# Kernel optimization log

Measured on AMD Instinct MI355X. Metric: run time of the kernel, lower is better.

Reference implementation:

```python
import jax, jax.numpy as jnp
import numpy as np

N, E, F_IN, D, H, G, T = 30000, 480000, 128, 32, 4, 128, 10
HD = H * D
NEG_SLOPE = 0.2


def _lin(key, fan_out, fan_in, scale=0.05):
    k1, k2 = jax.random.split(key)
    return (jax.random.normal(k1, (fan_out, fan_in), jnp.float32) * scale,
            jax.random.normal(k2, (fan_out,), jnp.float32) * scale)


def setup_inputs() -> dict:
    key = jax.random.key(0)
    ks = jax.random.split(key, 24)
    x = jax.random.normal(ks[0], (N, F_IN), jnp.float32)
    edge_index = jax.random.randint(ks[1], (2, E), 0, N, jnp.int64)
    batch = jnp.sort(jax.random.randint(ks[2], (N,), 0, G, jnp.int64))
    inp = {"x": x, "edge_index": edge_index, "batch": batch}
    # conv 0 (in=F_IN) and conv 1 (in=D); each followed by Linear(HD -> D)
    for i, fin in enumerate([F_IN, D]):
        base = 3 + i * 8
        Wl, bl = _lin(ks[base + 0], HD, fin)
        Wr, br = _lin(ks[base + 1], HD, fin)
        att = jax.random.normal(ks[base + 2], (H, D), jnp.float32) * 0.05
        bias = jnp.zeros((HD,), jnp.float32)
        lw, lb = _lin(ks[base + 3], D, HD)
        inp.update({f"Wl{i}": Wl, f"bl{i}": bl, f"Wr{i}": Wr, f"br{i}": br,
                    f"att{i}": att, f"cb{i}": bias, f"lw{i}": lw, f"lb{i}": lb})
    inp["fc1_W"], inp["fc1_b"] = _lin(ks[20], D, D)
    inp["fc2_W"], inp["fc2_b"] = _lin(ks[21], T, D)
    return inp


def _gatv2_conv(x, src, dst, Wl, bl, Wr, br, att, bias):
    # PyG GATv2Conv, concat=True, add_self_loops already applied to src/dst,
    # aggr='mean', eval mode (no dropout).
    n = x.shape[0]
    xl = (x @ Wl.T + bl).reshape(n, H, D)
    xr = (x @ Wr.T + br).reshape(n, H, D)
    e = jax.nn.leaky_relu(xl[src] + xr[dst], NEG_SLOPE)          # [E', H, D]
    alpha = jnp.einsum('ehd,hd->eh', e, att)                      # [E', H]
    amax = jax.ops.segment_max(alpha, dst, num_segments=n)        # [n, H]
    ex = jnp.exp(alpha - amax[dst])
    denom = jax.ops.segment_sum(ex, dst, num_segments=n)
    a = ex / denom[dst]                                           # softmax per target
    msg = xl[src] * a[:, :, None]                                 # [E', H, D]
    s = jax.ops.segment_sum(msg, dst, num_segments=n)
    cnt = jax.ops.segment_sum(jnp.ones((src.shape[0],), jnp.float32), dst, num_segments=n)
    out = s / cnt[:, None, None]                                  # mean aggregation
    return out.reshape(n, HD) + bias


def reference(x, edge_index, batch,
              Wl0, bl0, Wr0, br0, att0, cb0, lw0, lb0,
              Wl1, bl1, Wr1, br1, att1, cb1, lw1, lb1,
              fc1_W, fc1_b, fc2_W, fc2_b):
    loop = jnp.arange(N, dtype=edge_index.dtype)
    src = jnp.concatenate([edge_index[0], loop])  # add self loops
    dst = jnp.concatenate([edge_index[1], loop])
    convs = [(Wl0, bl0, Wr0, br0, att0, cb0, lw0, lb0),
             (Wl1, bl1, Wr1, br1, att1, cb1, lw1, lb1)]
    h = x
    for (Wl, bl, Wr, br, att, cb, lw, lb) in convs:
        h = _gatv2_conv(h, src, dst, Wl, bl, Wr, br, att, cb)
        h = h @ lw.T + lb  # heads>1: Linear(H*D -> D)
    g = jax.ops.segment_max(h, batch, num_segments=G)  # global max pool
    g = jax.nn.relu(g @ fc1_W.T + fc1_b)
    return g @ fc2_W.T + fc2_b
```

## Files before the change

### kernel.cpp

```cpp
#include <hip/hip_runtime.h>
#include <hip/hip_bf16.h>

#define NEG_SLOPE 0.2f
#define GGRP 128
#define TOUT 10

__global__ void init_kernel(int* __restrict__ deg, float* __restrict__ gpool,
                            int n, int gsize) {
    int i = blockIdx.x * blockDim.x + threadIdx.x;
    if (i < n) deg[i] = 0;
    if (i < gsize) gpool[i] = -__builtin_inff();
}

__global__ void degree_kernel(const int* __restrict__ dst, int* __restrict__ deg, int E) {
    int e = blockIdx.x * blockDim.x + threadIdx.x;
    if (e < E) atomicAdd(&deg[dst[e]], 1);
}

__global__ __launch_bounds__(256)
void scanA_kernel(const int* __restrict__ deg, int* __restrict__ rowptr,
                  int* __restrict__ bsum, int n) {
    __shared__ int wsum[4];
    int tid = threadIdx.x, lane = tid & 63, wid = tid >> 6;
    int idx = blockIdx.x * 256 + tid;
    int v = (idx < n) ? deg[idx] : 0;
    int x = v;
    #pragma unroll
    for (int off = 1; off < 64; off <<= 1) {
        int t = __shfl_up(x, off, 64);
        if (lane >= off) x += t;
    }
    if (lane == 63) wsum[wid] = x;
    __syncthreads();
    if (tid == 0) {
        int s = 0;
        #pragma unroll
        for (int i = 0; i < 4; ++i) { int t = wsum[i]; wsum[i] = s; s += t; }
        bsum[blockIdx.x] = s;
    }
    __syncthreads();
    int excl = x - v + wsum[wid];
    if (idx < n) rowptr[idx] = excl;
}

__global__ void scanB_kernel(const int* __restrict__ bsum, int* __restrict__ boff,
                             int* __restrict__ rowptr, int n, int nb) {
    int lane = threadIdx.x;
    int v0 = (lane < nb) ? bsum[lane] : 0;
    int v1 = (64 + lane < nb) ? bsum[64 + lane] : 0;
    int s0 = v0, s1 = v1;
    #pragma unroll
    for (int off = 1; off < 64; off <<= 1) {
        int t0 = __shfl_up(s0, off, 64);
        int t1 = __shfl_up(s1, off, 64);
        if (lane >= off) { s0 += t0; s1 += t1; }
    }
    int tot0 = __shfl(s0, 63, 64);
    s1 += tot0;
    boff[lane] = s0 - v0;
    boff[64 + lane] = s1 - v1;
    if (lane == 63) rowptr[n] = s1;
}

__global__ void scanC_kernel(int* __restrict__ rowptr, int* __restrict__ cursor,
                             const int* __restrict__ boff, int n) {
    int idx = blockIdx.x * blockDim.x + threadIdx.x;
    if (idx < n) {
        int r = rowptr[idx] + boff[idx >> 8];
        rowptr[idx] = r;
        cursor[idx] = r;
    }
}

__global__ void scatter_kernel(const int* __restrict__ src, const int* __restrict__ dst,
                               int* __restrict__ cursor, int* __restrict__ csr, int E) {
    int e = blockIdx.x * blockDim.x + threadIdx.x;
    if (e < E) {
        int slot = atomicAdd(&cursor[dst[e]], 1);
        csr[slot] = src[e];
    }
}

template <int FIN>
__global__ __launch_bounds__(256)
void gemm_xlxr_kernel(const float* __restrict__ X,
                      const float* __restrict__ Wl, const float* __restrict__ bl,
                      const float* __restrict__ Wr, const float* __restrict__ br,
                      float* __restrict__ xl, float* __restrict__ xr) {
    __shared__ float Wls[128][36];
    __shared__ float Wrs[128][36];
    __shared__ float Xs[16][36];
    int tid = threadIdx.x;
    int rowBase = blockIdx.x * 16;
    int c = tid & 127;
    int rs = tid >> 7;
    float accL[8] = {0.f}, accR[8] = {0.f};
    for (int k0 = 0; k0 < FIN; k0 += 32) {
        #pragma unroll
        for (int i = 0; i < 16; ++i) {
            int idx = tid + i * 256;
            int cc = idx >> 5, kk = idx & 31;
            Wls[cc][kk] = Wl[cc * FIN + k0 + kk];
            Wrs[cc][kk] = Wr[cc * FIN + k0 + kk];
        }
        #pragma unroll
        for (int i = 0; i < 2; ++i) {
            int idx = tid + i * 256;
            int r = idx >> 5, kk = idx & 31;
            Xs[r][kk] = X[(rowBase + r) * FIN + k0 + kk];
        }
        __syncthreads();
        #pragma unroll
        for (int k4 = 0; k4 < 32; k4 += 4) {
            float4 wl4 = *(const float4*)&Wls[c][k4];
            float4 wr4 = *(const float4*)&Wrs[c][k4];
            #pragma unroll
            for (int j = 0; j < 8; ++j) {
                float4 xv = *(const float4*)&Xs[rs * 8 + j][k4];
                accL[j] = fmaf(xv.x, wl4.x, accL[j]);
                accL[j] = fmaf(xv.y, wl4.y, accL[j]);
                accL[j] = fmaf(xv.z, wl4.z, accL[j]);
                accL[j] = fmaf(xv.w, wl4.w, accL[j]);
                accR[j] = fmaf(xv.x, wr4.x, accR[j]);
                accR[j] = fmaf(xv.y, wr4.y, accR[j]);
                accR[j] = fmaf(xv.z, wr4.z, accR[j]);
                accR[j] = fmaf(xv.w, wr4.w, accR[j]);
            }
        }
        __syncthreads();
    }
    float blv = bl[c], brv = br[c];
    #pragma unroll
    for (int j = 0; j < 8; ++j) {
        int row = rowBase + rs * 8 + j;
        xl[row * 128 + c] = accL[j] + blv;
        xr[row * 128 + c] = accR[j] + brv;
    }
}

__global__ __launch_bounds__(256)
void gat_fused_kernel(const float* __restrict__ xl, const float* __restrict__ xr,
                      const float* __restrict__ att, const float* __restrict__ cb,
                      const float* __restrict__ lw, const float* __restrict__ lb,
                      const int* __restrict__ rowptr, const int* __restrict__ csr,
                      float* __restrict__ out , int n) {
    __shared__ float lws[32][132];
    __shared__ float oslot[4][128];
    int tid = threadIdx.x;
    #pragma unroll
    for (int i = 0; i < 16; ++i) {
        int idx = tid + i * 256;
        lws[idx >> 7][idx & 127] = lw[idx];
    }
    __syncthreads();

    int wid = tid >> 6, lane = tid & 63;
    int nd = blockIdx.x * 4 + wid;
    if (nd >= n) return;
    int half = lane >> 5;
    int l32 = lane & 31;
    int f4 = l32 * 4;

    const float4 xr4  = *(const float4*)(xr + nd * 128 + f4);
    const float4 at4  = *(const float4*)(att + f4);
    const float4 xls4 = *(const float4*)(xl + nd * 128 + f4);

    int start = rowptr[nd], end = rowptr[nd + 1];

    float den;
    float4 acc;
    {
        float e0 = xls4.x + xr4.x; e0 = e0 > 0.f ? e0 : NEG_SLOPE * e0;
        float e1 = xls4.y + xr4.y; e1 = e1 > 0.f ? e1 : NEG_SLOPE * e1;
        float e2 = xls4.z + xr4.z; e2 = e2 > 0.f ? e2 : NEG_SLOPE * e2;
        float e3 = xls4.w + xr4.w; e3 = e3 > 0.f ? e3 : NEG_SLOPE * e3;
        float q = e0 * at4.x + e1 * at4.y + e2 * at4.z + e3 * at4.w;
        q += __shfl_xor(q, 1); q += __shfl_xor(q, 2); q += __shfl_xor(q, 4);
        float a = __expf(q);
        if (half == 0) {
            den = a;
            acc.x = a * xls4.x; acc.y = a * xls4.y;
            acc.z = a * xls4.z; acc.w = a * xls4.w;
        } else {
            den = 0.f; acc.x = acc.y = acc.z = acc.w = 0.f;
        }
    }

    for (int i = start + half; i < end; i += 2) {
        int s = csr[i];
        float4 xv = *(const float4*)(xl + (size_t)s * 128 + f4);
        float e0 = xv.x + xr4.x; e0 = e0 > 0.f ? e0 : NEG_SLOPE * e0;
        float e1 = xv.y + xr4.y; e1 = e1 > 0.f ? e1 : NEG_SLOPE * e1;
        float e2 = xv.z + xr4.z; e2 = e2 > 0.f ? e2 : NEG_SLOPE * e2;
        float e3 = xv.w + xr4.w; e3 = e3 > 0.f ? e3 : NEG_SLOPE * e3;
        float q = e0 * at4.x + e1 * at4.y + e2 * at4.z + e3 * at4.w;
        q += __shfl_xor(q, 1); q += __shfl_xor(q, 2); q += __shfl_xor(q, 4);
        float a = __expf(q);
        den += a;
        acc.x = fmaf(a, xv.x, acc.x);
        acc.y = fmaf(a, xv.y, acc.y);
        acc.z = fmaf(a, xv.z, acc.z);
        acc.w = fmaf(a, xv.w, acc.w);
    }

    acc.x += __shfl_xor(acc.x, 32);
    acc.y += __shfl_xor(acc.y, 32);
    acc.z += __shfl_xor(acc.z, 32);
    acc.w += __shfl_xor(acc.w, 32);
    den   += __shfl_xor(den, 32);

    float inv = 1.0f / (den * (float)(end - start + 1));
    const float4 cb4 = *(const float4*)(cb + f4);
    float4 o;
    o.x = fmaf(acc.x, inv, cb4.x);
    o.y = fmaf(acc.y, inv, cb4.y);
    o.z = fmaf(acc.z, inv, cb4.z);
    o.w = fmaf(acc.w, inv, cb4.w);

    if (half == 0) *(float4*)&oslot[wid][f4] = o;
    asm volatile("s_waitcnt lgkmcnt(0)" ::: "memory");

    float y = 0.f;
    int kbase = half * 64;
    #pragma unroll
    for (int k = 0; k < 64; k += 4) {
        float4 lv = *(const float4*)&lws[l32][kbase + k];
        float4 ov = *(const float4*)&oslot[wid][kbase + k];
        y = fmaf(lv.x, ov.x, y);
        y = fmaf(lv.y, ov.y, y);
        y = fmaf(lv.z, ov.z, y);
        y = fmaf(lv.w, ov.w, y);
    }
    y += __shfl_xor(y, 32);
    if (half == 0) out[nd * 32 + l32] = y + lb[l32];
}

__device__ __forceinline__ void atomicMaxFloat(float* addr, float val) {
    if (val >= 0.f) atomicMax((int*)addr, __float_as_int(val));
    else atomicMin((unsigned int*)addr, (unsigned int)__float_as_int(val));
}

__global__ void pool_kernel(const float* __restrict__ H, const int* __restrict__ batch,
                            float* __restrict__ g, int n) {
    int tid = threadIdx.x;
    int dim = tid & 31;
    int sub = tid >> 5;
    int nodeStart = blockIdx.x * 128 + sub * 16;
    float m = -__builtin_inff();
    int cur = -1;
    for (int j = 0; j < 16; ++j) {
        int nd = nodeStart + j;
        if (nd >= n) break;
        int b = batch[nd];
        if (b != cur) {
            if (cur >= 0) atomicMaxFloat(&g[cur * 32 + dim], m);
            cur = b; m = -__builtin_inff();
        }
        m = fmaxf(m, H[nd * 32 + dim]);
    }
    if (cur >= 0) atomicMaxFloat(&g[cur * 32 + dim], m);
}

__global__ __launch_bounds__(256)
void fc_kernel(const float* __restrict__ g,
               const float* __restrict__ fc1W, const float* __restrict__ fc1b,
               const float* __restrict__ fc2W, const float* __restrict__ fc2b,
               float* __restrict__ out) {
    __shared__ float g1[GGRP * 32];
    int tid = threadIdx.x;
    for (int idx = tid; idx < GGRP * 32; idx += 256) {
        int r = idx >> 5, c = idx & 31;
        float acc = fc1b[c];
        #pragma unroll
        for (int k = 0; k < 32; ++k) acc = fmaf(g[r * 32 + k], fc1W[c * 32 + k], acc);
        g1[idx] = acc > 0.f ? acc : 0.f;
    }
    __syncthreads();
    for (int idx = tid; idx < GGRP * TOUT; idx += 256) {
        int r = idx / TOUT, c = idx - r * TOUT;
        float acc = fc2b[c];
        #pragma unroll
        for (int k = 0; k < 32; ++k) acc = fmaf(g1[r * 32 + k], fc2W[c * 32 + k], acc);
        out[idx] = acc;
    }
}

extern "C" void kernel_launch(void* const* d_in, const int* in_sizes, int n_in,
                              void* d_out, int out_size, void* d_ws, size_t ws_size,
                              hipStream_t stream) {
    const float* x     = (const float*)d_in[0];
    const int*   ei    = (const int*)d_in[1];
    const int*   batch = (const int*)d_in[2];
    const float* Wl0 = (const float*)d_in[3];
    const float* bl0 = (const float*)d_in[4];
    const float* Wr0 = (const float*)d_in[5];
    const float* br0 = (const float*)d_in[6];
    const float* at0 = (const float*)d_in[7];
    const float* cb0 = (const float*)d_in[8];
    const float* lw0 = (const float*)d_in[9];
    const float* lb0 = (const float*)d_in[10];
    const float* Wl1 = (const float*)d_in[11];
    const float* bl1 = (const float*)d_in[12];
    const float* Wr1 = (const float*)d_in[13];
    const float* br1 = (const float*)d_in[14];
    const float* at1 = (const float*)d_in[15];
    const float* cb1 = (const float*)d_in[16];
    const float* lw1 = (const float*)d_in[17];
    const float* lb1 = (const float*)d_in[18];
    const float* fc1W = (const float*)d_in[19];
    const float* fc1b = (const float*)d_in[20];
    const float* fc2W = (const float*)d_in[21];
    const float* fc2b = (const float*)d_in[22];

    const int n = in_sizes[0] / 128;
    const int E = in_sizes[1] / 2;
    const int* src = ei;
    const int* dst = ei + E;
    const int nblkScan = (n + 255) / 256;

    size_t off = 0;
    auto alloc = [&](size_t bytes) {
        void* p = (char*)d_ws + off;
        off += (bytes + 255) & ~(size_t)255;
        return p;
    };
    float* xl    = (float*)alloc((size_t)n * 128 * 4);
    float* xr    = (float*)alloc((size_t)n * 128 * 4);
    float* hbuf  = (float*)alloc((size_t)n * 32 * 4);
    int* deg     = (int*)alloc((size_t)n * 4);
    int* rowptr  = (int*)alloc((size_t)(n + 1) * 4);
    int* cursor  = (int*)alloc((size_t)n * 4);
    int* csr     = (int*)alloc((size_t)E * 4);
    int* bsum    = (int*)alloc(128 * 4);
    int* boff    = (int*)alloc(128 * 4);
    float* gpool = (float*)alloc((size_t)GGRP * 32 * 4);

    init_kernel<<<(n + 255) / 256, 256, 0, stream>>>(deg, gpool, n, GGRP * 32);
    degree_kernel<<<(E + 255) / 256, 256, 0, stream>>>(dst, deg, E);
    scanA_kernel<<<nblkScan, 256, 0, stream>>>(deg, rowptr, bsum, n);
    scanB_kernel<<<1, 64, 0, stream>>>(bsum, boff, rowptr, n, nblkScan);
    scanC_kernel<<<nblkScan, 256, 0, stream>>>(rowptr, cursor, boff, n);
    scatter_kernel<<<(E + 255) / 256, 256, 0, stream>>>(src, dst, cursor, csr, E);

    gemm_xlxr_kernel<128><<<n / 16, 256, 0, stream>>>(x, Wl0, bl0, Wr0, br0, xl, xr);
    gat_fused_kernel<<<(n + 3) / 4, 256, 0, stream>>>(xl, xr, at0, cb0, lw0, lb0,
                                                      rowptr, csr, hbuf, n);
    gemm_xlxr_kernel<32><<<n / 16, 256, 0, stream>>>(hbuf, Wl1, bl1, Wr1, br1, xl, xr);
    gat_fused_kernel<<<(n + 3) / 4, 256, 0, stream>>>(xl, xr, at1, cb1, lw1, lb1,
                                                      rowptr, csr, hbuf, n);

    pool_kernel<<<(n + 127) / 128, 256, 0, stream>>>(hbuf, batch, gpool, n);
    fc_kernel<<<1, 256, 0, stream>>>(gpool, fc1W, fc1b, fc2W, fc2b, (float*)d_out);
}
```

Before: 345.2 us.

## Retile xl/xr GEMM into column blocks and prefetch neighbor gathers in GAT

```diff
diff --git a/kernel.cpp b/kernel.cpp
--- a/kernel.cpp
+++ b/kernel.cpp
@@ -86,55 +86,53 @@
 void gemm_xlxr_kernel(const float* __restrict__ X,
                       const float* __restrict__ Wl, const float* __restrict__ bl,
                       const float* __restrict__ Wr, const float* __restrict__ br,
-                      float* __restrict__ xl, float* __restrict__ xr) {
-    __shared__ float Wls[128][36];
-    __shared__ float Wrs[128][36];
-    __shared__ float Xs[16][36];
+                      float* __restrict__ xl, float* __restrict__ xr, int n) {
+    constexpr int KP = FIN + 4;
+    __shared__ float Ws[64][KP];
+    __shared__ float Xs[32][KP];
     int tid = threadIdx.x;
-    int rowBase = blockIdx.x * 16;
-    int c = tid & 127;
-    int rs = tid >> 7;
-    float accL[8] = {0.f}, accR[8] = {0.f};
-    for (int k0 = 0; k0 < FIN; k0 += 32) {
+    int nRowBlk = (n + 31) >> 5;
+    int rowBlk = blockIdx.x % nRowBlk;
+    int colBlk = blockIdx.x / nRowBlk;
+    const float* Wbase = (colBlk < 2) ? Wl : Wr;
+    const float* bbase = (colBlk < 2) ? bl : br;
+    float*       obase = (colBlk < 2) ? xl : xr;
+    int cOff = (colBlk & 1) * 64;
+    int row0 = rowBlk * 32;
+
+    for (int idx = tid * 4; idx < 64 * FIN; idx += 1024) {
+        int r = idx / FIN, k = idx % FIN;
+        *(float4*)&Ws[r][k] = *(const float4*)&Wbase[(cOff + r) * FIN + k];
+    }
+    for (int idx = tid * 4; idx < 32 * FIN; idx += 1024) {
+        int r = idx / FIN, k = idx % FIN;
+        int gr = row0 + r;
+        float4 v = {0.f, 0.f, 0.f, 0.f};
+        if (gr < n) v = *(const float4*)&X[(size_t)gr * FIN + k];
+        *(float4*)&Xs[r][k] = v;
+    }
+    __syncthreads();
+
+    int cc = tid & 63;
+    int rg = tid >> 6;
+    float acc[8] = {0.f, 0.f, 0.f, 0.f, 0.f, 0.f, 0.f, 0.f};
+    #pragma unroll 4
+    for (int k = 0; k < FIN; k += 4) {
+        float4 w4 = *(const float4*)&Ws[cc][k];
         #pragma unroll
-        for (int i = 0; i < 16; ++i) {
-            int idx = tid + i * 256;
-            int cc = idx >> 5, kk = idx & 31;
-            Wls[cc][kk] = Wl[cc * FIN + k0 + kk];
-            Wrs[cc][kk] = Wr[cc * FIN + k0 + kk];
+        for (int j = 0; j < 8; ++j) {
+            float4 x4 = *(const float4*)&Xs[rg * 8 + j][k];
+            acc[j] = fmaf(x4.x, w4.x, acc[j]);
+            acc[j] = fmaf(x4.y, w4.y, acc[j]);
+            acc[j] = fmaf(x4.z, w4.z, acc[j]);
+            acc[j] = fmaf(x4.w, w4.w, acc[j]);
         }
-        #pragma unroll
-        for (int i = 0; i < 2; ++i) {
-            int idx = tid + i * 256;
-            int r = idx >> 5, kk = idx & 31;
-            Xs[r][kk] = X[(rowBase + r) * FIN + k0 + kk];
-        }
-        __syncthreads();
-        #pragma unroll
-        for (int k4 = 0; k4 < 32; k4 += 4) {
-            float4 wl4 = *(const float4*)&Wls[c][k4];
-            float4 wr4 = *(const float4*)&Wrs[c][k4];
-            #pragma unroll
-            for (int j = 0; j < 8; ++j) {
-                float4 xv = *(const float4*)&Xs[rs * 8 + j][k4];
-                accL[j] = fmaf(xv.x, wl4.x, accL[j]);
-                accL[j] = fmaf(xv.y, wl4.y, accL[j]);
-                accL[j] = fmaf(xv.z, wl4.z, accL[j]);
-                accL[j] = fmaf(xv.w, wl4.w, accL[j]);
-                accR[j] = fmaf(xv.x, wr4.x, accR[j]);
-                accR[j] = fmaf(xv.y, wr4.y, accR[j]);
-                accR[j] = fmaf(xv.z, wr4.z, accR[j]);
-                accR[j] = fmaf(xv.w, wr4.w, accR[j]);
-            }
-        }
-        __syncthreads();
-    }
-    float blv = bl[c], brv = br[c];
+    }
+    float bv = bbase[cOff + cc];
     #pragma unroll
     for (int j = 0; j < 8; ++j) {
-        int row = rowBase + rs * 8 + j;
-        xl[row * 128 + c] = accL[j] + blv;
-        xr[row * 128 + c] = accR[j] + brv;
+        int gr = row0 + rg * 8 + j;
+        if (gr < n) obase[(size_t)gr * 128 + cOff + cc] = acc[j] + bv;
     }
 }
 
@@ -161,9 +159,9 @@
     int l32 = lane & 31;
     int f4 = l32 * 4;
 
-    const float4 xr4  = *(const float4*)(xr + nd * 128 + f4);
+    const float4 xr4  = *(const float4*)(xr + (size_t)nd * 128 + f4);
     const float4 at4  = *(const float4*)(att + f4);
-    const float4 xls4 = *(const float4*)(xl + nd * 128 + f4);
+    const float4 xls4 = *(const float4*)(xl + (size_t)nd * 128 + f4);
 
     int start = rowptr[nd], end = rowptr[nd + 1];
 
@@ -186,9 +184,16 @@
         }
     }
 
-    for (int i = start + half; i < end; i += 2) {
-        int s = csr[i];
-        float4 xv = *(const float4*)(xl + (size_t)s * 128 + f4);
+    int i = start + half;
+    int sA = (i < end) ? csr[i] : 0;
+    int sB = (i + 2 < end) ? csr[i + 2] : 0;
+    float4 xvA = {0.f, 0.f, 0.f, 0.f};
+    if (i < end) xvA = *(const float4*)(xl + (size_t)sA * 128 + f4);
+    for (; i < end; i += 2) {
+        float4 xv = xvA;
+        sA = sB;
+        if (i + 4 < end) sB = csr[i + 4];
+        if (i + 2 < end) xvA = *(const float4*)(xl + (size_t)sA * 128 + f4);
         float e0 = xv.x + xr4.x; e0 = e0 > 0.f ? e0 : NEG_SLOPE * e0;
         float e1 = xv.y + xr4.y; e1 = e1 > 0.f ? e1 : NEG_SLOPE * e1;
         float e2 = xv.z + xr4.z; e2 = e2 > 0.f ? e2 : NEG_SLOPE * e2;
@@ -232,7 +237,7 @@
         y = fmaf(lv.w, ov.w, y);
     }
     y += __shfl_xor(y, 32);
-    if (half == 0) out[nd * 32 + l32] = y + lb[l32];
+    if (half == 0) out[(size_t)nd * 32 + l32] = y + lb[l32];
 }
 
 __device__ __forceinline__ void atomicMaxFloat(float* addr, float val) {
@@ -317,6 +322,7 @@
     const int* src = ei;
     const int* dst = ei + E;
     const int nblkScan = (n + 255) / 256;
+    const int nRowBlk = (n + 31) / 32;
 
     size_t off = 0;
     auto alloc = [&](size_t bytes) {
@@ -342,10 +348,10 @@
     scanC_kernel<<<nblkScan, 256, 0, stream>>>(rowptr, cursor, boff, n);
     scatter_kernel<<<(E + 255) / 256, 256, 0, stream>>>(src, dst, cursor, csr, E);
 
-    gemm_xlxr_kernel<128><<<n / 16, 256, 0, stream>>>(x, Wl0, bl0, Wr0, br0, xl, xr);
+    gemm_xlxr_kernel<128><<<4 * nRowBlk, 256, 0, stream>>>(x, Wl0, bl0, Wr0, br0, xl, xr, n);
     gat_fused_kernel<<<(n + 3) / 4, 256, 0, stream>>>(xl, xr, at0, cb0, lw0, lb0,
                                                       rowptr, csr, hbuf, n);
-    gemm_xlxr_kernel<32><<<n / 16, 256, 0, stream>>>(hbuf, Wl1, bl1, Wr1, br1, xl, xr);
+    gemm_xlxr_kernel<32><<<4 * nRowBlk, 256, 0, stream>>>(hbuf, Wl1, bl1, Wr1, br1, xl, xr, n);
     gat_fused_kernel<<<(n + 3) / 4, 256, 0, stream>>>(xl, xr, at1, cb1, lw1, lb1,
                                                       rowptr, csr, hbuf, n);
 
```

New measurement: 346.8 us. About the same (+0.5%).

## Use 128x128 register-tiled GEMM and 4-way edge-parallel prefetching GAT aggregation

Applied to the files above, without the earlier changes.

```diff
diff --git a/kernel.cpp b/kernel.cpp
--- a/kernel.cpp
+++ b/kernel.cpp
@@ -82,59 +82,104 @@
 }
 
 template <int FIN>
-__global__ __launch_bounds__(256)
-void gemm_xlxr_kernel(const float* __restrict__ X,
+__global__ __launch_bounds__(256, 2)
+void gemm_tile_kernel(const float* __restrict__ X,
                       const float* __restrict__ Wl, const float* __restrict__ bl,
                       const float* __restrict__ Wr, const float* __restrict__ br,
-                      float* __restrict__ xl, float* __restrict__ xr) {
-    __shared__ float Wls[128][36];
-    __shared__ float Wrs[128][36];
-    __shared__ float Xs[16][36];
+                      float* __restrict__ xl, float* __restrict__ xr,
+                      int n, int nRowBlk) {
+    constexpr int BK = 32, BM = 128, LDA = BM + 4;
+    constexpr int NCHUNK = FIN / BK;
+    __shared__ float Xs[BK][LDA];
+    __shared__ float Ws[BK][LDA];
     int tid = threadIdx.x;
-    int rowBase = blockIdx.x * 16;
-    int c = tid & 127;
-    int rs = tid >> 7;
-    float accL[8] = {0.f}, accR[8] = {0.f};
-    for (int k0 = 0; k0 < FIN; k0 += 32) {
-        #pragma unroll
-        for (int i = 0; i < 16; ++i) {
-            int idx = tid + i * 256;
-            int cc = idx >> 5, kk = idx & 31;
-            Wls[cc][kk] = Wl[cc * FIN + k0 + kk];
-            Wrs[cc][kk] = Wr[cc * FIN + k0 + kk];
-        }
-        #pragma unroll
-        for (int i = 0; i < 2; ++i) {
-            int idx = tid + i * 256;
-            int r = idx >> 5, kk = idx & 31;
-            Xs[r][kk] = X[(rowBase + r) * FIN + k0 + kk];
-        }
-        __syncthreads();
-        #pragma unroll
-        for (int k4 = 0; k4 < 32; k4 += 4) {
-            float4 wl4 = *(const float4*)&Wls[c][k4];
-            float4 wr4 = *(const float4*)&Wrs[c][k4];
+    int rowBlk = blockIdx.x;
+    int colBlk = 0;
+    if (rowBlk >= nRowBlk) { rowBlk -= nRowBlk; colBlk = 1; }
+    const float* __restrict__ Wb = colBlk ? Wr : Wl;
+    const float* __restrict__ bb = colBlk ? br : bl;
+    float* __restrict__ ob = colBlk ? xr : xl;
+    int row0 = rowBlk * BM;
+
+    int sr  = tid >> 3;
+    int skq = (tid & 7) * 4;
+
+    float4 xpre[4], wpre[4];
+
+    auto load_pre = [&](int c) {
+        int k0 = c * BK;
+        #pragma unroll
+        for (int i = 0; i < 4; ++i) {
+            int r = sr + i * 32;
+            int gr = row0 + r;
+            float4 v = {0.f, 0.f, 0.f, 0.f};
+            if (gr < n) v = *(const float4*)&X[(size_t)gr * FIN + k0 + skq];
+            xpre[i] = v;
+            wpre[i] = *(const float4*)&Wb[(size_t)r * FIN + k0 + skq];
+        }
+    };
+    auto store_pre = [&]() {
+        #pragma unroll
+        for (int i = 0; i < 4; ++i) {
+            int r = sr + i * 32;
+            Xs[skq + 0][r] = xpre[i].x; Xs[skq + 1][r] = xpre[i].y;
+            Xs[skq + 2][r] = xpre[i].z; Xs[skq + 3][r] = xpre[i].w;
+            Ws[skq + 0][r] = wpre[i].x; Ws[skq + 1][r] = wpre[i].y;
+            Ws[skq + 2][r] = wpre[i].z; Ws[skq + 3][r] = wpre[i].w;
+        }
+    };
+
+    load_pre(0);
+    store_pre();
+    __syncthreads();
+
+    int tx = tid & 15;
+    int ty = tid >> 4;
+    float acc[8][8];
+    #pragma unroll
+    for (int i = 0; i < 8; ++i)
+        #pragma unroll
+        for (int j = 0; j < 8; ++j) acc[i][j] = 0.f;
+
+    #pragma unroll
+    for (int c = 0; c < NCHUNK; ++c) {
+        if (c + 1 < NCHUNK) load_pre(c + 1);
+        #pragma unroll 8
+        for (int k = 0; k < BK; ++k) {
+            float4 a0 = *(const float4*)&Xs[k][ty * 8];
+            float4 a1 = *(const float4*)&Xs[k][ty * 8 + 4];
+            float4 b0 = *(const float4*)&Ws[k][tx * 8];
+            float4 b1 = *(const float4*)&Ws[k][tx * 8 + 4];
+            float av[8] = {a0.x, a0.y, a0.z, a0.w, a1.x, a1.y, a1.z, a1.w};
+            float bv[8] = {b0.x, b0.y, b0.z, b0.w, b1.x, b1.y, b1.z, b1.w};
             #pragma unroll
-            for (int j = 0; j < 8; ++j) {
-                float4 xv = *(const float4*)&Xs[rs * 8 + j][k4];
-                accL[j] = fmaf(xv.x, wl4.x, accL[j]);
-                accL[j] = fmaf(xv.y, wl4.y, accL[j]);
-                accL[j] = fmaf(xv.z, wl4.z, accL[j]);
-                accL[j] = fmaf(xv.w, wl4.w, accL[j]);
-                accR[j] = fmaf(xv.x, wr4.x, accR[j]);
-                accR[j] = fmaf(xv.y, wr4.y, accR[j]);
-                accR[j] = fmaf(xv.z, wr4.z, accR[j]);
-                accR[j] = fmaf(xv.w, wr4.w, accR[j]);
-            }
-        }
-        __syncthreads();
-    }
-    float blv = bl[c], brv = br[c];
-    #pragma unroll
-    for (int j = 0; j < 8; ++j) {
-        int row = rowBase + rs * 8 + j;
-        xl[row * 128 + c] = accL[j] + blv;
-        xr[row * 128 + c] = accR[j] + brv;
+            for (int i = 0; i < 8; ++i)
+                #pragma unroll
+                for (int j = 0; j < 8; ++j)
+                    acc[i][j] = fmaf(av[i], bv[j], acc[i][j]);
+        }
+        if (c + 1 < NCHUNK) {
+            __syncthreads();
+            store_pre();
+            __syncthreads();
+        }
+    }
+
+    float bias[8];
+    #pragma unroll
+    for (int j = 0; j < 8; ++j) bias[j] = bb[tx * 8 + j];
+    #pragma unroll
+    for (int i = 0; i < 8; ++i) {
+        int gr = row0 + ty * 8 + i;
+        if (gr < n) {
+            float4 o0, o1;
+            o0.x = acc[i][0] + bias[0]; o0.y = acc[i][1] + bias[1];
+            o0.z = acc[i][2] + bias[2]; o0.w = acc[i][3] + bias[3];
+            o1.x = acc[i][4] + bias[4]; o1.y = acc[i][5] + bias[5];
+            o1.z = acc[i][6] + bias[6]; o1.w = acc[i][7] + bias[7];
+            *(float4*)&ob[(size_t)gr * 128 + tx * 8]     = o0;
+            *(float4*)&ob[(size_t)gr * 128 + tx * 8 + 4] = o1;
+        }
     }
 }
 
@@ -157,69 +202,105 @@
     int wid = tid >> 6, lane = tid & 63;
     int nd = blockIdx.x * 4 + wid;
     if (nd >= n) return;
+    int q4  = lane >> 4;
+    int l16 = lane & 15;
+    int f8  = l16 * 8;
+
+    const float4 xrA  = *(const float4*)(xr + (size_t)nd * 128 + f8);
+    const float4 xrB  = *(const float4*)(xr + (size_t)nd * 128 + f8 + 4);
+    const float4 atA  = *(const float4*)(att + f8);
+    const float4 atB  = *(const float4*)(att + f8 + 4);
+    const float4 xlsA = *(const float4*)(xl + (size_t)nd * 128 + f8);
+    const float4 xlsB = *(const float4*)(xl + (size_t)nd * 128 + f8 + 4);
+
+    int start = rowptr[nd], end = rowptr[nd + 1];
+
+    float den;
+    float accA[4] = {0.f, 0.f, 0.f, 0.f};
+    float accB[4] = {0.f, 0.f, 0.f, 0.f};
+
+    {
+        float e0 = xlsA.x + xrA.x; e0 = e0 > 0.f ? e0 : NEG_SLOPE * e0;
+        float e1 = xlsA.y + xrA.y; e1 = e1 > 0.f ? e1 : NEG_SLOPE * e1;
+        float e2 = xlsA.z + xrA.z; e2 = e2 > 0.f ? e2 : NEG_SLOPE * e2;
+        float e3 = xlsA.w + xrA.w; e3 = e3 > 0.f ? e3 : NEG_SLOPE * e3;
+        float e4 = xlsB.x + xrB.x; e4 = e4 > 0.f ? e4 : NEG_SLOPE * e4;
+        float e5 = xlsB.y + xrB.y; e5 = e5 > 0.f ? e5 : NEG_SLOPE * e5;
+        float e6 = xlsB.z + xrB.z; e6 = e6 > 0.f ? e6 : NEG_SLOPE * e6;
+        float e7 = xlsB.w + xrB.w; e7 = e7 > 0.f ? e7 : NEG_SLOPE * e7;
+        float q = e0 * atA.x + e1 * atA.y + e2 * atA.z + e3 * atA.w
+                + e4 * atB.x + e5 * atB.y + e6 * atB.z + e7 * atB.w;
+        q += __shfl_xor(q, 1); q += __shfl_xor(q, 2);
+        float a = __expf(q);
+        if (q4 == 0) {
+            den = a;
+            accA[0] = a * xlsA.x; accA[1] = a * xlsA.y;
+            accA[2] = a * xlsA.z; accA[3] = a * xlsA.w;
+            accB[0] = a * xlsB.x; accB[1] = a * xlsB.y;
+            accB[2] = a * xlsB.z; accB[3] = a * xlsB.w;
+        } else {
+            den = 0.f;
+        }
+    }
+
+    int i = start + q4;
+    int sA = (i < end) ? csr[i] : 0;
+    int sB = (i + 4 < end) ? csr[i + 4] : 0;
+    float4 pre0 = {0.f, 0.f, 0.f, 0.f}, pre1 = pre0;
+    if (i < end) {
+        pre0 = *(const float4*)(xl + (size_t)sA * 128 + f8);
+        pre1 = *(const float4*)(xl + (size_t)sA * 128 + f8 + 4);
+    }
+    for (; i < end; i += 4) {
+        float4 x0 = pre0, x1 = pre1;
+        sA = sB;
+        if (i + 8 < end) sB = csr[i + 8];
+        if (i + 4 < end) {
+            pre0 = *(const float4*)(xl + (size_t)sA * 128 + f8);
+            pre1 = *(const float4*)(xl + (size_t)sA * 128 + f8 + 4);
+        }
+        float e0 = x0.x + xrA.x; e0 = e0 > 0.f ? e0 : NEG_SLOPE * e0;
+        float e1 = x0.y + xrA.y; e1 = e1 > 0.f ? e1 : NEG_SLOPE * e1;
+        float e2 = x0.z + xrA.z; e2 = e2 > 0.f ? e2 : NEG_SLOPE * e2;
+        float e3 = x0.w + xrA.w; e3 = e3 > 0.f ? e3 : NEG_SLOPE * e3;
+        float e4 = x1.x + xrB.x; e4 = e4 > 0.f ? e4 : NEG_SLOPE * e4;
+        float e5 = x1.y + xrB.y; e5 = e5 > 0.f ? e5 : NEG_SLOPE * e5;
+        float e6 = x1.z + xrB.z; e6 = e6 > 0.f ? e6 : NEG_SLOPE * e6;
+        float e7 = x1.w + xrB.w; e7 = e7 > 0.f ? e7 : NEG_SLOPE * e7;
+        float q = e0 * atA.x + e1 * atA.y + e2 * atA.z + e3 * atA.w
+                + e4 * atB.x + e5 * atB.y + e6 * atB.z + e7 * atB.w;
+        q += __shfl_xor(q, 1); q += __shfl_xor(q, 2);
+        float a = __expf(q);
+        den += a;
+        accA[0] = fmaf(a, x0.x, accA[0]); accA[1] = fmaf(a, x0.y, accA[1]);
+        accA[2] = fmaf(a, x0.z, accA[2]); accA[3] = fmaf(a, x0.w, accA[3]);
+        accB[0] = fmaf(a, x1.x, accB[0]); accB[1] = fmaf(a, x1.y, accB[1]);
+        accB[2] = fmaf(a, x1.z, accB[2]); accB[3] = fmaf(a, x1.w, accB[3]);
+    }
+
+    #pragma unroll
+    for (int j = 0; j < 4; ++j) {
+        accA[j] += __shfl_xor(accA[j], 16); accA[j] += __shfl_xor(accA[j], 32);
+        accB[j] += __shfl_xor(accB[j], 16); accB[j] += __shfl_xor(accB[j], 32);
+    }
+    den += __shfl_xor(den, 16); den += __shfl_xor(den, 32);
+
+    float inv = 1.0f / (den * (float)(end - start + 1));
+    if (q4 == 0) {
+        const float4 cbA = *(const float4*)(cb + f8);
+        const float4 cbB = *(const float4*)(cb + f8 + 4);
+        float4 oA, oB;
+        oA.x = fmaf(accA[0], inv, cbA.x); oA.y = fmaf(accA[1], inv, cbA.y);
+        oA.z = fmaf(accA[2], inv, cbA.z); oA.w = fmaf(accA[3], inv, cbA.w);
+        oB.x = fmaf(accB[0], inv, cbB.x); oB.y = fmaf(accB[1], inv, cbB.y);
+        oB.z = fmaf(accB[2], inv, cbB.z); oB.w = fmaf(accB[3], inv, cbB.w);
+        *(float4*)&oslot[wid][f8]     = oA;
+        *(float4*)&oslot[wid][f8 + 4] = oB;
+    }
+    asm volatile("s_waitcnt lgkmcnt(0)" ::: "memory");
+
     int half = lane >> 5;
     int l32 = lane & 31;
-    int f4 = l32 * 4;
-
-    const float4 xr4  = *(const float4*)(xr + nd * 128 + f4);
-    const float4 at4  = *(const float4*)(att + f4);
-    const float4 xls4 = *(const float4*)(xl + nd * 128 + f4);
-
-    int start = rowptr[nd], end = rowptr[nd + 1];
-
-    float den;
-    float4 acc;
-    {
-        float e0 = xls4.x + xr4.x; e0 = e0 > 0.f ? e0 : NEG_SLOPE * e0;
-        float e1 = xls4.y + xr4.y; e1 = e1 > 0.f ? e1 : NEG_SLOPE * e1;
-        float e2 = xls4.z + xr4.z; e2 = e2 > 0.f ? e2 : NEG_SLOPE * e2;
-        float e3 = xls4.w + xr4.w; e3 = e3 > 0.f ? e3 : NEG_SLOPE * e3;
-        float q = e0 * at4.x + e1 * at4.y + e2 * at4.z + e3 * at4.w;
-        q += __shfl_xor(q, 1); q += __shfl_xor(q, 2); q += __shfl_xor(q, 4);
-        float a = __expf(q);
-        if (half == 0) {
-            den = a;
-            acc.x = a * xls4.x; acc.y = a * xls4.y;
-            acc.z = a * xls4.z; acc.w = a * xls4.w;
-        } else {
-            den = 0.f; acc.x = acc.y = acc.z = acc.w = 0.f;
-        }
-    }
-
-    for (int i = start + half; i < end; i += 2) {
-        int s = csr[i];
-        float4 xv = *(const float4*)(xl + (size_t)s * 128 + f4);
-        float e0 = xv.x + xr4.x; e0 = e0 > 0.f ? e0 : NEG_SLOPE * e0;
-        float e1 = xv.y + xr4.y; e1 = e1 > 0.f ? e1 : NEG_SLOPE * e1;
-        float e2 = xv.z + xr4.z; e2 = e2 > 0.f ? e2 : NEG_SLOPE * e2;
-        float e3 = xv.w + xr4.w; e3 = e3 > 0.f ? e3 : NEG_SLOPE * e3;
-        float q = e0 * at4.x + e1 * at4.y + e2 * at4.z + e3 * at4.w;
-        q += __shfl_xor(q, 1); q += __shfl_xor(q, 2); q += __shfl_xor(q, 4);
-        float a = __expf(q);
-        den += a;
-        acc.x = fmaf(a, xv.x, acc.x);
-        acc.y = fmaf(a, xv.y, acc.y);
-        acc.z = fmaf(a, xv.z, acc.z);
-        acc.w = fmaf(a, xv.w, acc.w);
-    }
-
-    acc.x += __shfl_xor(acc.x, 32);
-    acc.y += __shfl_xor(acc.y, 32);
-    acc.z += __shfl_xor(acc.z, 32);
-    acc.w += __shfl_xor(acc.w, 32);
-    den   += __shfl_xor(den, 32);
-
-    float inv = 1.0f / (den * (float)(end - start + 1));
-    const float4 cb4 = *(const float4*)(cb + f4);
-    float4 o;
-    o.x = fmaf(acc.x, inv, cb4.x);
-    o.y = fmaf(acc.y, inv, cb4.y);
-    o.z = fmaf(acc.z, inv, cb4.z);
-    o.w = fmaf(acc.w, inv, cb4.w);
-
-    if (half == 0) *(float4*)&oslot[wid][f4] = o;
-    asm volatile("s_waitcnt lgkmcnt(0)" ::: "memory");
-
     float y = 0.f;
     int kbase = half * 64;
     #pragma unroll
@@ -232,7 +313,7 @@
         y = fmaf(lv.w, ov.w, y);
     }
     y += __shfl_xor(y, 32);
-    if (half == 0) out[nd * 32 + l32] = y + lb[l32];
+    if (half == 0) out[(size_t)nd * 32 + l32] = y + lb[l32];
 }
 
 __device__ __forceinline__ void atomicMaxFloat(float* addr, float val) {
@@ -317,6 +398,7 @@
     const int* src = ei;
     const int* dst = ei + E;
     const int nblkScan = (n + 255) / 256;
+    const int nRowBlk = (n + 127) / 128;
 
     size_t off = 0;
     auto alloc = [&](size_t bytes) {
@@ -342,10 +424,12 @@
     scanC_kernel<<<nblkScan, 256, 0, stream>>>(rowptr, cursor, boff, n);
     scatter_kernel<<<(E + 255) / 256, 256, 0, stream>>>(src, dst, cursor, csr, E);
 
-    gemm_xlxr_kernel<128><<<n / 16, 256, 0, stream>>>(x, Wl0, bl0, Wr0, br0, xl, xr);
+    gemm_tile_kernel<128><<<2 * nRowBlk, 256, 0, stream>>>(x, Wl0, bl0, Wr0, br0,
+                                                           xl, xr, n, nRowBlk);
     gat_fused_kernel<<<(n + 3) / 4, 256, 0, stream>>>(xl, xr, at0, cb0, lw0, lb0,
                                                       rowptr, csr, hbuf, n);
-    gemm_xlxr_kernel<32><<<n / 16, 256, 0, stream>>>(hbuf, Wl1, bl1, Wr1, br1, xl, xr);
+    gemm_tile_kernel<32><<<2 * nRowBlk, 256, 0, stream>>>(hbuf, Wl1, bl1, Wr1, br1,
+                                                          xl, xr, n, nRowBlk);
     gat_fused_kernel<<<(n + 3) / 4, 256, 0, stream>>>(xl, xr, at1, cb1, lw1, lb1,
                                                       rowptr, csr, hbuf, n);
 
```

After: 311.7 us. 9.7% less time.
